# Optimization experiments

Measured on AMD Instinct MI355X. Metric: run time of the kernel, lower is better.

## Reference

```python
import jax, jax.numpy as jnp
import numpy as np

T, B, I, H = 1024, 64, 512, 512


def flip_batch(data, lengths):
    # data: [T, B, D]; reverse the first lengths[i] timesteps of each batch column i.
    t = jnp.arange(data.shape[0])[:, None]                 # [T, 1]
    L = lengths[None, :]                                   # [1, B]
    idx = jnp.where(t < L, L - 1 - t, t)                   # [T, B]
    return jnp.take_along_axis(data, idx[:, :, None], axis=0)


def lstm_scan(x, h0, c0, w_ih, w_hh, b):
    # x: [T, B, I]; standard torch LSTMCell math, gate order (i, f, g, o).
    def step(carry, xt):
        h, c = carry
        gates = xt @ w_ih.T + h @ w_hh.T + b               # [B, 4H]
        i, f, g, o = jnp.split(gates, 4, axis=-1)
        i = jax.nn.sigmoid(i)
        f = jax.nn.sigmoid(f)
        g = jnp.tanh(g)
        o = jax.nn.sigmoid(o)
        c = f * c + i * g
        h = o * jnp.tanh(c)
        return (h, c), h

    (_, _), ys = jax.lax.scan(step, (h0, c0), x)
    return ys                                              # [T, B, H]


def setup_inputs() -> dict:
    key = jax.random.key(0)
    ks = jax.random.split(key, 16)
    s = 0.05
    return {
        "input": jax.random.normal(ks[0], (T, B, I), jnp.float32),
        "lengths": jax.random.randint(ks[1], (B,), 0, T),
        "h0_f": jax.random.normal(ks[2], (B, H), jnp.float32) * s,
        "c0_f": jax.random.normal(ks[3], (B, H), jnp.float32) * s,
        "h0_b": jax.random.normal(ks[4], (B, H), jnp.float32) * s,
        "c0_b": jax.random.normal(ks[5], (B, H), jnp.float32) * s,
        "w_ih_f": jax.random.normal(ks[6], (4 * H, I), jnp.float32) * s,
        "w_hh_f": jax.random.normal(ks[7], (4 * H, H), jnp.float32) * s,
        "b_ih_f": jax.random.normal(ks[8], (4 * H,), jnp.float32) * s,
        "b_hh_f": jax.random.normal(ks[9], (4 * H,), jnp.float32) * s,
        "w_ih_b": jax.random.normal(ks[10], (4 * H, I), jnp.float32) * s,
        "w_hh_b": jax.random.normal(ks[11], (4 * H, H), jnp.float32) * s,
        "b_ih_b": jax.random.normal(ks[12], (4 * H,), jnp.float32) * s,
        "b_hh_b": jax.random.normal(ks[13], (4 * H,), jnp.float32) * s,
    }


def reference(input, lengths, h0_f, c0_f, h0_b, c0_b,
              w_ih_f, w_hh_f, b_ih_f, b_hh_f,
              w_ih_b, w_hh_b, b_ih_b, b_hh_b):
    # Forward-direction layer: plain left-to-right scan over full sequence.
    out_f = lstm_scan(input, h0_f, c0_f, w_ih_f, w_hh_f, b_ih_f + b_hh_f)
    # Backward layer with length-aware reversal (flipBatch), then flip outputs back.
    x_rev = flip_batch(input, lengths)
    ys = lstm_scan(x_rev, h0_b, c0_b, w_ih_b, w_hh_b, b_ih_b + b_hh_b)
    out_b = flip_batch(ys, lengths)
    # lengths provided => module returns (concat, None); return the output tensor.
    return jnp.concatenate([out_f, out_b], axis=-1)       # [T, B, 2H]
```

## Files before the change

kernel.cpp:

```cpp
#include <hip/hip_runtime.h>
#include <hip/hip_bf16.h>

#define T_LEN  1024
#define BATCH  64
#define HDIM   512
#define G4     2048

typedef __attribute__((ext_vector_type(8))) short short8;
typedef __attribute__((ext_vector_type(4))) float f32x4;
typedef __attribute__((ext_vector_type(4))) unsigned int u32x4;
typedef __hip_bfloat16 bf16;

__device__ __forceinline__ unsigned short bfbits(float f) {
    bf16 h = __float2bfloat16(f);
    return __builtin_bit_cast(unsigned short, h);
}
__device__ __forceinline__ float fsigmoid(float x) { return 1.f / (1.f + __expf(-x)); }
__device__ __forceinline__ float ftanh(float x)    { return 2.f / (1.f + __expf(-2.f * x)) - 1.f; }

__global__ void conv_weights(const float* __restrict__ wihf, const float* __restrict__ whhf,
                             const float* __restrict__ bihf, const float* __restrict__ bhhf,
                             const float* __restrict__ wihb, const float* __restrict__ whhb,
                             const float* __restrict__ bihb, const float* __restrict__ bhhb,
                             bf16* __restrict__ wih, bf16* __restrict__ whh,
                             float* __restrict__ bias)
{
    int i = blockIdx.x * 256 + threadIdx.x;
    const int n1 = G4 * HDIM;
    if (i < n1) {
        wih[i] = __float2bfloat16(wihf[i]);
        whh[i] = __float2bfloat16(whhf[i]);
    } else {
        int k = i - n1;
        wih[n1 + k] = __float2bfloat16(wihb[k]);
        whh[n1 + k] = __float2bfloat16(whhb[k]);
    }
    if (i < G4)          bias[i] = bihf[i] + bhhf[i];
    else if (i < 2 * G4) bias[i] = bihb[i - G4] + bhhb[i - G4];
}

__global__ void conv_x(const float* __restrict__ x, bf16* __restrict__ xb)
{
    size_t i = (size_t)blockIdx.x * 256 + threadIdx.x;
    const float* s = x + i * 8;
    float4 a = *reinterpret_cast<const float4*>(s);
    float4 b = *reinterpret_cast<const float4*>(s + 4);
    union { unsigned short us[8]; u32x4 v; } p;
    p.us[0] = bfbits(a.x); p.us[1] = bfbits(a.y); p.us[2] = bfbits(a.z); p.us[3] = bfbits(a.w);
    p.us[4] = bfbits(b.x); p.us[5] = bfbits(b.y); p.us[6] = bfbits(b.z); p.us[7] = bfbits(b.w);
    *reinterpret_cast<u32x4*>(xb + i * 8) = p.v;
}

__global__ void init_state(const float* __restrict__ h0f, const float* __restrict__ c0f,
                           const float* __restrict__ h0b, const float* __restrict__ c0b,
                           bf16* __restrict__ hbuf, float* __restrict__ cbuf,
                           unsigned* __restrict__ flags, unsigned* __restrict__ xcdarr,
                           unsigned* __restrict__ abortw)
{
    int i = blockIdx.x * 256 + threadIdx.x;
    int d = i >> 15, r = i & 32767;
    const float* h0 = d ? h0b : h0f;
    const float* c0 = d ? c0b : c0f;
    hbuf[(0 * 2 + d) * (BATCH * HDIM) + r] = __float2bfloat16(h0[r]);
    cbuf[d * (BATCH * HDIM) + r] = c0[r];
    if (blockIdx.x == 0) {
        flags[threadIdx.x]  = 0;
        xcdarr[threadIdx.x] = 0;
        if (threadIdx.x == 0) *abortw = 0;
    }
}

__global__ __launch_bounds__(256, 1) void lstm_full(
        const bf16* __restrict__ xb,
        const bf16* __restrict__ wih,
        const bf16* __restrict__ whh,
        const float* __restrict__ bias,
        const int*  __restrict__ lengths,
        bf16*       __restrict__ hbuf,
        float*      __restrict__ cbuf,
        float*      __restrict__ out,
        unsigned*   __restrict__ flags,
        unsigned*   __restrict__ xcdarr,
        unsigned*   __restrict__ abortw)
{
    __shared__ __align__(16) char Wl[64 * 2048];
    __shared__ __align__(16) char Al[16 * 1024];
    __shared__ float Gl[16][68];
    __shared__ int ok_sh;

    const int tid  = threadIdx.x;
    const int team = (int)blockIdx.x & 7;
    const int rank = (int)blockIdx.x >> 3;
    const int dir  = team >> 2;
    const int b0   = (team & 3) * 16;
    const int u0   = rank * 16;
    const int lane = tid & 63;
    const int w    = tid >> 6;

    if (tid == 0) {
        unsigned xcc;
        asm volatile("s_getreg_b32 %0, hwreg(20, 0, 32)" : "=s"(xcc));
        __hip_atomic_store(&xcdarr[blockIdx.x], (xcc & 0xFu) + 1u,
                           __ATOMIC_RELAXED, __HIP_MEMORY_SCOPE_SYSTEM);
    }

    {
        const bf16* wihd = wih + (size_t)dir * G4 * HDIM;
        const bf16* whhd = whh + (size_t)dir * G4 * HDIM;
#pragma unroll
        for (int i = 0; i < 32; i++) {
            int q = tid + i * 256;
            int c = q >> 7, s = q & 127;
            int grow = (c >> 4) * HDIM + u0 + (c & 15);
            const bf16* src = (s < 64) ? (wihd + (size_t)grow * HDIM + s * 8)
                                       : (whhd + (size_t)grow * HDIM + (s - 64) * 8);
            u32x4 v = *reinterpret_cast<const u32x4*>(src);
            *reinterpret_cast<u32x4*>(&Wl[(c * 2048 + s * 16) ^ ((c & 7) << 4)]) = v;
        }
    }

    if (rank == 0) {
        if (w == 0) {
            int idx = (lane < 32) ? (team + lane * 8) : ((team ^ 1) + (lane - 32) * 8);
            const unsigned* p = xcdarr + idx;
            unsigned v = 0, cnt = 0; int timeout = 0;
            for (;;) {
                v = __hip_atomic_load(p, __ATOMIC_RELAXED, __HIP_MEMORY_SCOPE_SYSTEM);
                if (__all((int)((v & 31u) != 0u))) break;
                if (++cnt > (1u << 20)) { timeout = 1; break; }
            }
            unsigned my = (unsigned)__shfl((int)(v & 31u), 0);
            int ok = (!timeout) &&
                     __all(lane < 32 ? (int)((v & 31u) == my) : (int)((v & 31u) != my));
            if (ok && lane < 32)
                __hip_atomic_store(&flags[team * 32 + lane], 0u,
                                   __ATOMIC_RELAXED, __HIP_MEMORY_SCOPE_WORKGROUP);
            asm volatile("s_waitcnt vmcnt(0)" ::: "memory");
            if (lane == 0) {
                unsigned pub = my | 32u | (ok ? 64u : 0u);
                __hip_atomic_store(&xcdarr[blockIdx.x], pub,
                                   __ATOMIC_RELAXED, __HIP_MEMORY_SCOPE_SYSTEM);
                ok_sh = ok;
            }
        }
    } else {
        if (tid == 0) {
            const unsigned* p = xcdarr + team;
            unsigned v;
            do {
                v = __hip_atomic_load(p, __ATOMIC_RELAXED, __HIP_MEMORY_SCOPE_SYSTEM);
            } while (!(v & 32u));
            ok_sh = (int)((v >> 6) & 1u);
        }
    }

    const int bb = tid >> 4;
    const int uu = tid & 15;
    const int b_glob = b0 + bb;
    const int Lb = lengths[b_glob];
    float c_reg = __hip_atomic_load(&cbuf[((size_t)dir * BATCH + b_glob) * HDIM + u0 + uu],
                                    __ATOMIC_RELAXED, __HIP_MEMORY_SCOPE_SYSTEM);
    float bias_r[4];
#pragma unroll
    for (int g = 0; g < 4; g++)
        bias_r[g] = bias[dir * G4 + g * HDIM + u0 + uu];
    int Lw[4];
#pragma unroll
    for (int i = 0; i < 4; i++) Lw[i] = lengths[b0 + i * 4 + w];

    const int arow  = lane & 15;
    const int axor  = (arow & 7) << 4;
    const int abase = arow * 1024;
    const int brow  = w * 16 + (lane & 15);
    const int bxor  = (brow & 7) << 4;
    const int bbase = brow * 2048;
    const int kbhi  = (lane >> 4) * 16;

    unsigned* flagw = flags + team * 32 + rank;
    const unsigned* pollp = flags + team * 32 + (lane & 31);

    __syncthreads();
    const bool fast = (ok_sh != 0);

    for (int t = 0; t < T_LEN; ++t) {
        const int p = t & 1;

#pragma unroll
        for (int i = 0; i < 4; i++) {
            int row = i * 4 + w;
            int st = t;
            if (dir) { int L = Lw[i]; st = (t < L) ? (L - 1 - t) : t; }
            u32x4 v = *reinterpret_cast<const u32x4*>(
                xb + ((size_t)st * BATCH + b0 + row) * HDIM + lane * 8);
            *reinterpret_cast<u32x4*>(&Al[(row * 1024 + lane * 16) ^ ((row & 7) << 4)]) = v;
        }
        __syncthreads();

        f32x4 acc = f32x4{0.f, 0.f, 0.f, 0.f};
#pragma unroll
        for (int ks = 0; ks < 16; ++ks) {
            int kb = ks * 64 + kbhi;
            short8 a = *reinterpret_cast<const short8*>(&Al[(abase + kb) ^ axor]);
            short8 b = *reinterpret_cast<const short8*>(&Wl[(bbase + kb) ^ bxor]);
            acc = __builtin_amdgcn_mfma_f32_16x16x32_bf16(a, b, acc, 0, 0, 0);
        }

        if (w == 0 && t > 0) {
            unsigned token = (unsigned)t, v, cnt = 0;
            if (fast) {
                for (;;) {
                    asm volatile("global_load_dword %0, %1, off sc0\n\ts_waitcnt vmcnt(0)"
                                 : "=v"(v) : "v"(pollp) : "memory");
                    if (__all((int)(v >= token))) break;
                    if (((++cnt) & 4095u) == 0) {
                        if (__hip_atomic_load(abortw, __ATOMIC_RELAXED, __HIP_MEMORY_SCOPE_SYSTEM)) break;
                        if (cnt > (1u << 22)) {
                            __hip_atomic_store(abortw, 1u, __ATOMIC_RELAXED, __HIP_MEMORY_SCOPE_SYSTEM);
                            break;
                        }
                    }
                }
            } else {
                for (;;) {
                    v = __hip_atomic_load(pollp, __ATOMIC_RELAXED, __HIP_MEMORY_SCOPE_SYSTEM);
                    if (__all((int)(v >= token))) break;
                    if (((++cnt) & 4095u) == 0) {
                        if (__hip_atomic_load(abortw, __ATOMIC_RELAXED, __HIP_MEMORY_SCOPE_SYSTEM)) break;
                        if (cnt > (1u << 22)) {
                            __hip_atomic_store(abortw, 1u, __ATOMIC_RELAXED, __HIP_MEMORY_SCOPE_SYSTEM);
                            break;
                        }
                    }
                }
            }
        }
        __syncthreads();

        {
            const bf16* hb = hbuf + ((size_t)(p * 2 + dir) * BATCH + b0) * HDIM;
            if (fast && t > 0) {
                u32x4 h4[4];
#pragma unroll
                for (int i = 0; i < 4; i++) {
                    int row = i * 4 + w;
                    const bf16* hp = hb + (size_t)row * HDIM + lane * 8;
                    asm volatile("global_load_dwordx4 %0, %1, off sc0"
                                 : "=v"(h4[i]) : "v"(hp) : "memory");
                }
                asm volatile("s_waitcnt vmcnt(0)" ::: "memory");
#pragma unroll
                for (int i = 0; i < 4; i++) {
                    int row = i * 4 + w;
                    *reinterpret_cast<u32x4*>(&Al[(row * 1024 + lane * 16) ^ ((row & 7) << 4)]) = h4[i];
                }
            } else {
#pragma unroll
                for (int i = 0; i < 8; i++) {
                    int q = tid + i * 256;
                    int row = q >> 7, sb = (q & 127) * 8;
                    unsigned long long v = __hip_atomic_load(
                        reinterpret_cast<const unsigned long long*>(hb) + q,
                        __ATOMIC_RELAXED, __HIP_MEMORY_SCOPE_SYSTEM);
                    *reinterpret_cast<unsigned long long*>(
                        &Al[(row * 1024 + sb) ^ ((row & 7) << 4)]) = v;
                }
            }
        }
        __syncthreads();

#pragma unroll
        for (int ks = 0; ks < 16; ++ks) {
            int kb = ks * 64 + kbhi;
            short8 a = *reinterpret_cast<const short8*>(&Al[(abase + kb) ^ axor]);
            short8 b = *reinterpret_cast<const short8*>(&Wl[(bbase + 1024 + kb) ^ bxor]);
            acc = __builtin_amdgcn_mfma_f32_16x16x32_bf16(a, b, acc, 0, 0, 0);
        }

        {
            int col = w * 16 + (lane & 15);
            int rb  = (lane >> 4) * 4;
#pragma unroll
            for (int r = 0; r < 4; r++) Gl[rb + r][col] = acc[r];
        }
        __syncthreads();

        float gi = Gl[bb][uu]      + bias_r[0];
        float gf = Gl[bb][16 + uu] + bias_r[1];
        float gg = Gl[bb][32 + uu] + bias_r[2];
        float go = Gl[bb][48 + uu] + bias_r[3];
        float iv = fsigmoid(gi), fv = fsigmoid(gf), gv = ftanh(gg), ov = fsigmoid(go);
        c_reg = fv * c_reg + iv * gv;
        float hv = ov * ftanh(c_reg);

        unsigned lo = (unsigned)bfbits(hv);
        unsigned hi = (unsigned)__shfl_down((int)lo, 1);
        if ((uu & 1) == 0) {
            unsigned* hw = reinterpret_cast<unsigned*>(
                hbuf + (size_t)((p ^ 1) * 2 + dir) * BATCH * HDIM) + ((b_glob * HDIM + u0 + uu) >> 1);
            unsigned val = lo | (hi << 16);
            if (fast) __hip_atomic_store(hw, val, __ATOMIC_RELAXED, __HIP_MEMORY_SCOPE_WORKGROUP);
            else      __hip_atomic_store(hw, val, __ATOMIC_RELAXED, __HIP_MEMORY_SCOPE_SYSTEM);
        }
        int tout = t;
        if (dir) tout = (t < Lb) ? (Lb - 1 - t) : t;
        out[((size_t)tout * BATCH + b_glob) * (2 * HDIM) + dir * HDIM + u0 + uu] = hv;

        __syncthreads();
        if (tid == 0) {
            unsigned tok = (unsigned)(t + 1);
            if (fast) __hip_atomic_store(flagw, tok, __ATOMIC_RELAXED, __HIP_MEMORY_SCOPE_WORKGROUP);
            else      __hip_atomic_store(flagw, tok, __ATOMIC_RELAXED, __HIP_MEMORY_SCOPE_SYSTEM);
        }
    }

    cbuf[((size_t)dir * BATCH + b_glob) * HDIM + u0 + uu] = c_reg;
}

extern "C" void kernel_launch(void* const* d_in, const int* in_sizes, int n_in,
                              void* d_out, int out_size, void* d_ws, size_t ws_size,
                              hipStream_t stream)
{
    const float* x     = (const float*)d_in[0];
    const int* lengths = (const int*)d_in[1];
    const float* h0f   = (const float*)d_in[2];
    const float* c0f   = (const float*)d_in[3];
    const float* h0b   = (const float*)d_in[4];
    const float* c0b   = (const float*)d_in[5];
    const float* wihf  = (const float*)d_in[6];
    const float* whhf  = (const float*)d_in[7];
    const float* bihf  = (const float*)d_in[8];
    const float* bhhf  = (const float*)d_in[9];
    const float* wihb  = (const float*)d_in[10];
    const float* whhb  = (const float*)d_in[11];
    const float* bihb  = (const float*)d_in[12];
    const float* bhhb  = (const float*)d_in[13];
    float* out = (float*)d_out;

    char* ws = (char*)d_ws;
    bf16*     wih_bf = (bf16*)(ws);
    bf16*     whh_bf = (bf16*)(ws + (4u << 20));
    float*    bias   = (float*)(ws + (8u << 20));
    bf16*     hbuf   = (bf16*)(ws + (9u << 20));
    float*    cbuf   = (float*)(ws + (10u << 20));
    unsigned* flags  = (unsigned*)(ws + (11u << 20));
    unsigned* xcdarr = (unsigned*)(ws + (11u << 20) + 4096);
    unsigned* abortw = (unsigned*)(ws + (11u << 20) + 8192);
    bf16*     xb     = (bf16*)(ws + (16u << 20));

    conv_weights<<<dim3(2 * G4 * HDIM / 256), dim3(256), 0, stream>>>(
        wihf, whhf, bihf, bhhf, wihb, whhb, bihb, bhhb, wih_bf, whh_bf, bias);
    conv_x<<<dim3((T_LEN * BATCH * HDIM / 8) / 256), dim3(256), 0, stream>>>(x, xb);
    init_state<<<dim3(2 * BATCH * HDIM / 256), dim3(256), 0, stream>>>(
        h0f, c0f, h0b, c0b, hbuf, cbuf, flags, xcdarr, abortw);

    lstm_full<<<dim3(256), dim3(256), 0, stream>>>(
        xb, wih_bf, whh_bf, bias, lengths, hbuf, cbuf, out, flags, xcdarr, abortw);
}
```

Before: 2.488 ms.

## Keep LSTM weights in registers and prefetch next-step inputs before the barrier

Each wave now holds its slices of the input and recurrent weights in VGPRs (short8 fragments) instead of staging them in LDS. It computes the input projection before polling for the previous hidden state, and loads h and x directly from global memory into MFMA operands instead of going through LDS. The next timestep's x is prefetched after the recurrent MFMAs, and the bias is folded into the accumulator init. h0/c0 are read directly, which removes the init_state kernel and the cbuf buffer. A 100KB LDS pad keeps one block per CU. The aim is to take LDS round-trips and a barrier off the serial recurrent critical path, at the cost of much higher register pressure.

Measured after the change: 4.543 ms. 1.83x slower.

```diff
diff --git a/kernel.cpp b/kernel.cpp
--- a/kernel.cpp
+++ b/kernel.cpp
@@ -51,23 +51,13 @@
     *reinterpret_cast<u32x4*>(xb + i * 8) = p.v;
 }
 
-__global__ void init_state(const float* __restrict__ h0f, const float* __restrict__ c0f,
-                           const float* __restrict__ h0b, const float* __restrict__ c0b,
-                           bf16* __restrict__ hbuf, float* __restrict__ cbuf,
-                           unsigned* __restrict__ flags, unsigned* __restrict__ xcdarr,
-                           unsigned* __restrict__ abortw)
-{
-    int i = blockIdx.x * 256 + threadIdx.x;
-    int d = i >> 15, r = i & 32767;
-    const float* h0 = d ? h0b : h0f;
-    const float* c0 = d ? c0b : c0f;
-    hbuf[(0 * 2 + d) * (BATCH * HDIM) + r] = __float2bfloat16(h0[r]);
-    cbuf[d * (BATCH * HDIM) + r] = c0[r];
-    if (blockIdx.x == 0) {
-        flags[threadIdx.x]  = 0;
-        xcdarr[threadIdx.x] = 0;
-        if (threadIdx.x == 0) *abortw = 0;
-    }
+__global__ void init_sync(unsigned* __restrict__ flags, unsigned* __restrict__ xcdarr,
+                          unsigned* __restrict__ abortw)
+{
+    int i = threadIdx.x;
+    __hip_atomic_store(&flags[i],  0u, __ATOMIC_RELAXED, __HIP_MEMORY_SCOPE_SYSTEM);
+    __hip_atomic_store(&xcdarr[i], 0u, __ATOMIC_RELAXED, __HIP_MEMORY_SCOPE_SYSTEM);
+    if (i == 0) __hip_atomic_store(abortw, 0u, __ATOMIC_RELAXED, __HIP_MEMORY_SCOPE_SYSTEM);
 }
 
 __global__ __launch_bounds__(256, 1) void lstm_full(
@@ -76,17 +66,17 @@
         const bf16* __restrict__ whh,
         const float* __restrict__ bias,
         const int*  __restrict__ lengths,
+        const float* __restrict__ h0f, const float* __restrict__ c0f,
+        const float* __restrict__ h0b, const float* __restrict__ c0b,
         bf16*       __restrict__ hbuf,
-        float*      __restrict__ cbuf,
         float*      __restrict__ out,
         unsigned*   __restrict__ flags,
         unsigned*   __restrict__ xcdarr,
         unsigned*   __restrict__ abortw)
 {
-    __shared__ __align__(16) char Wl[64 * 2048];
-    __shared__ __align__(16) char Al[16 * 1024];
     __shared__ float Gl[16][68];
     __shared__ int ok_sh;
+    __shared__ char lds_pad[100000];
 
     const int tid  = threadIdx.x;
     const int team = (int)blockIdx.x & 7;
@@ -96,27 +86,16 @@
     const int u0   = rank * 16;
     const int lane = tid & 63;
     const int w    = tid >> 6;
+    const int uu   = lane & 15;
+    const int q    = lane >> 4;
+
+    ((volatile char*)lds_pad)[tid] = 1;
 
     if (tid == 0) {
         unsigned xcc;
         asm volatile("s_getreg_b32 %0, hwreg(20, 0, 32)" : "=s"(xcc));
         __hip_atomic_store(&xcdarr[blockIdx.x], (xcc & 0xFu) + 1u,
                            __ATOMIC_RELAXED, __HIP_MEMORY_SCOPE_SYSTEM);
-    }
-
-    {
-        const bf16* wihd = wih + (size_t)dir * G4 * HDIM;
-        const bf16* whhd = whh + (size_t)dir * G4 * HDIM;
-#pragma unroll
-        for (int i = 0; i < 32; i++) {
-            int q = tid + i * 256;
-            int c = q >> 7, s = q & 127;
-            int grow = (c >> 4) * HDIM + u0 + (c & 15);
-            const bf16* src = (s < 64) ? (wihd + (size_t)grow * HDIM + s * 8)
-                                       : (whhd + (size_t)grow * HDIM + (s - 64) * 8);
-            u32x4 v = *reinterpret_cast<const u32x4*>(src);
-            *reinterpret_cast<u32x4*>(&Wl[(c * 2048 + s * 16) ^ ((c & 7) << 4)]) = v;
-        }
     }
 
     if (rank == 0) {
@@ -132,9 +111,11 @@
             unsigned my = (unsigned)__shfl((int)(v & 31u), 0);
             int ok = (!timeout) &&
                      __all(lane < 32 ? (int)((v & 31u) == my) : (int)((v & 31u) != my));
-            if (ok && lane < 32)
-                __hip_atomic_store(&flags[team * 32 + lane], 0u,
+            if (ok && lane < 32) {
+                unsigned old = __hip_atomic_exchange(&flags[team * 32 + lane], 0u,
                                    __ATOMIC_RELAXED, __HIP_MEMORY_SCOPE_WORKGROUP);
+                (void)old;
+            }
             asm volatile("s_waitcnt vmcnt(0)" ::: "memory");
             if (lane == 0) {
                 unsigned pub = my | 32u | (ok ? 64u : 0u);
@@ -146,66 +127,63 @@
     } else {
         if (tid == 0) {
             const unsigned* p = xcdarr + team;
-            unsigned v;
-            do {
+            unsigned v, cnt = 0;
+            for (;;) {
                 v = __hip_atomic_load(p, __ATOMIC_RELAXED, __HIP_MEMORY_SCOPE_SYSTEM);
-            } while (!(v & 32u));
+                if (v & 32u) break;
+                if (++cnt > (1u << 24)) { v = 32u; break; }
+            }
             ok_sh = (int)((v >> 6) & 1u);
         }
     }
 
+    short8 BI[16], BH[16];
+    {
+        const size_t grow = (size_t)(w * HDIM + u0 + uu);
+        const bf16* wi = wih + (size_t)dir * G4 * HDIM + grow * HDIM + q * 8;
+        const bf16* wh = whh + (size_t)dir * G4 * HDIM + grow * HDIM + q * 8;
+#pragma unroll
+        for (int ks = 0; ks < 16; ++ks) {
+            BI[ks] = *reinterpret_cast<const short8*>(wi + ks * 32);
+            BH[ks] = *reinterpret_cast<const short8*>(wh + ks * 32);
+        }
+    }
+    const float bs = bias[dir * G4 + w * HDIM + u0 + uu];
+
     const int bb = tid >> 4;
-    const int uu = tid & 15;
+    const int cu = tid & 15;
     const int b_glob = b0 + bb;
     const int Lb = lengths[b_glob];
-    float c_reg = __hip_atomic_load(&cbuf[((size_t)dir * BATCH + b_glob) * HDIM + u0 + uu],
-                                    __ATOMIC_RELAXED, __HIP_MEMORY_SCOPE_SYSTEM);
-    float bias_r[4];
-#pragma unroll
-    for (int g = 0; g < 4; g++)
-        bias_r[g] = bias[dir * G4 + g * HDIM + u0 + uu];
-    int Lw[4];
-#pragma unroll
-    for (int i = 0; i < 4; i++) Lw[i] = lengths[b0 + i * 4 + w];
-
-    const int arow  = lane & 15;
-    const int axor  = (arow & 7) << 4;
-    const int abase = arow * 1024;
-    const int brow  = w * 16 + (lane & 15);
-    const int bxor  = (brow & 7) << 4;
-    const int bbase = brow * 2048;
-    const int kbhi  = (lane >> 4) * 16;
-
+    float c_reg = (dir ? c0b : c0f)[(size_t)b_glob * HDIM + u0 + cu];
+
+    const int LA = lengths[b0 + uu];
+
+    const unsigned* pollp = flags + team * 32 + (lane & 31);
     unsigned* flagw = flags + team * 32 + rank;
-    const unsigned* pollp = flags + team * 32 + (lane & 31);
 
     __syncthreads();
     const bool fast = (ok_sh != 0);
+    int dead = 0;
+
+    u32x4 A[16];
+    {
+        int st = 0; if (dir) st = (0 < LA) ? (LA - 1) : 0;
+        const bf16* xp = xb + ((size_t)st * BATCH + b0 + uu) * HDIM + q * 8;
+#pragma unroll
+        for (int ks = 0; ks < 16; ++ks)
+            A[ks] = *reinterpret_cast<const u32x4*>(xp + ks * 32);
+    }
 
     for (int t = 0; t < T_LEN; ++t) {
         const int p = t & 1;
 
-#pragma unroll
-        for (int i = 0; i < 4; i++) {
-            int row = i * 4 + w;
-            int st = t;
-            if (dir) { int L = Lw[i]; st = (t < L) ? (L - 1 - t) : t; }
-            u32x4 v = *reinterpret_cast<const u32x4*>(
-                xb + ((size_t)st * BATCH + b0 + row) * HDIM + lane * 8);
-            *reinterpret_cast<u32x4*>(&Al[(row * 1024 + lane * 16) ^ ((row & 7) << 4)]) = v;
-        }
-        __syncthreads();
-
-        f32x4 acc = f32x4{0.f, 0.f, 0.f, 0.f};
-#pragma unroll
-        for (int ks = 0; ks < 16; ++ks) {
-            int kb = ks * 64 + kbhi;
-            short8 a = *reinterpret_cast<const short8*>(&Al[(abase + kb) ^ axor]);
-            short8 b = *reinterpret_cast<const short8*>(&Wl[(bbase + kb) ^ bxor]);
-            acc = __builtin_amdgcn_mfma_f32_16x16x32_bf16(a, b, acc, 0, 0, 0);
-        }
-
-        if (w == 0 && t > 0) {
+        f32x4 accx = f32x4{bs, bs, bs, bs};
+#pragma unroll
+        for (int ks = 0; ks < 16; ++ks)
+            accx = __builtin_amdgcn_mfma_f32_16x16x32_bf16(
+                __builtin_bit_cast(short8, A[ks]), BI[ks], accx, 0, 0, 0);
+
+        if (w == 0 && t > 0 && !dead) {
             unsigned token = (unsigned)t, v, cnt = 0;
             if (fast) {
                 for (;;) {
@@ -213,10 +191,10 @@
                                  : "=v"(v) : "v"(pollp) : "memory");
                     if (__all((int)(v >= token))) break;
                     if (((++cnt) & 4095u) == 0) {
-                        if (__hip_atomic_load(abortw, __ATOMIC_RELAXED, __HIP_MEMORY_SCOPE_SYSTEM)) break;
+                        if (__hip_atomic_load(abortw, __ATOMIC_RELAXED, __HIP_MEMORY_SCOPE_SYSTEM)) { dead = 1; break; }
                         if (cnt > (1u << 22)) {
                             __hip_atomic_store(abortw, 1u, __ATOMIC_RELAXED, __HIP_MEMORY_SCOPE_SYSTEM);
-                            break;
+                            dead = 1; break;
                         }
                     }
                 }
@@ -225,10 +203,10 @@
                     v = __hip_atomic_load(pollp, __ATOMIC_RELAXED, __HIP_MEMORY_SCOPE_SYSTEM);
                     if (__all((int)(v >= token))) break;
                     if (((++cnt) & 4095u) == 0) {
-                        if (__hip_atomic_load(abortw, __ATOMIC_RELAXED, __HIP_MEMORY_SCOPE_SYSTEM)) break;
+                        if (__hip_atomic_load(abortw, __ATOMIC_RELAXED, __HIP_MEMORY_SCOPE_SYSTEM)) { dead = 1; break; }
                         if (cnt > (1u << 22)) {
                             __hip_atomic_store(abortw, 1u, __ATOMIC_RELAXED, __HIP_MEMORY_SCOPE_SYSTEM);
-                            break;
+                            dead = 1; break;
                         }
                     }
                 }
@@ -236,84 +214,111 @@
         }
         __syncthreads();
 
+        u32x4 H[16];
+        if (t == 0) {
+            const float* h0p = (dir ? h0b : h0f) + (size_t)(b0 + uu) * HDIM;
+#pragma unroll
+            for (int ks = 0; ks < 16; ++ks) {
+                const float* s = h0p + ks * 32 + q * 8;
+                float4 f0 = *reinterpret_cast<const float4*>(s);
+                float4 f1 = *reinterpret_cast<const float4*>(s + 4);
+                union { unsigned short us[8]; u32x4 v; } pk;
+                pk.us[0] = bfbits(f0.x); pk.us[1] = bfbits(f0.y);
+                pk.us[2] = bfbits(f0.z); pk.us[3] = bfbits(f0.w);
+                pk.us[4] = bfbits(f1.x); pk.us[5] = bfbits(f1.y);
+                pk.us[6] = bfbits(f1.z); pk.us[7] = bfbits(f1.w);
+                H[ks] = pk.v;
+            }
+        } else {
+            const bf16* hb = hbuf + (size_t)(p * 2 + dir) * (BATCH * HDIM)
+                                  + (size_t)(b0 + uu) * HDIM + q * 8;
+            if (fast) {
+#pragma unroll
+                for (int ks = 0; ks < 16; ++ks)
+                    asm volatile("global_load_dwordx4 %0, %1, off sc0"
+                                 : "=v"(H[ks]) : "v"(hb + ks * 32) : "memory");
+                asm volatile("s_waitcnt vmcnt(0)" ::: "memory");
+                __builtin_amdgcn_sched_barrier(0);
+            } else {
+#pragma unroll
+                for (int ks = 0; ks < 16; ++ks) {
+                    union { unsigned long long qv[2]; u32x4 v; } pk;
+                    pk.qv[0] = __hip_atomic_load(
+                        reinterpret_cast<const unsigned long long*>(hb + ks * 32),
+                        __ATOMIC_RELAXED, __HIP_MEMORY_SCOPE_SYSTEM);
+                    pk.qv[1] = __hip_atomic_load(
+                        reinterpret_cast<const unsigned long long*>(hb + ks * 32 + 4),
+                        __ATOMIC_RELAXED, __HIP_MEMORY_SCOPE_SYSTEM);
+                    H[ks] = pk.v;
+                }
+            }
+        }
+
+        f32x4 acch0 = f32x4{0.f, 0.f, 0.f, 0.f};
+        f32x4 acch1 = f32x4{0.f, 0.f, 0.f, 0.f};
+#pragma unroll
+        for (int ks = 0; ks < 8; ++ks) {
+            acch0 = __builtin_amdgcn_mfma_f32_16x16x32_bf16(
+                __builtin_bit_cast(short8, H[2 * ks]),     BH[2 * ks],     acch0, 0, 0, 0);
+            acch1 = __builtin_amdgcn_mfma_f32_16x16x32_bf16(
+                __builtin_bit_cast(short8, H[2 * ks + 1]), BH[2 * ks + 1], acch1, 0, 0, 0);
+        }
+
+        if (t + 1 < T_LEN) {
+            int tn = t + 1, st = tn;
+            if (dir) st = (tn < LA) ? (LA - 1 - tn) : tn;
+            const bf16* xp = xb + ((size_t)st * BATCH + b0 + uu) * HDIM + q * 8;
+#pragma unroll
+            for (int ks = 0; ks < 16; ++ks)
+                A[ks] = *reinterpret_cast<const u32x4*>(xp + ks * 32);
+        }
+
         {
-            const bf16* hb = hbuf + ((size_t)(p * 2 + dir) * BATCH + b0) * HDIM;
-            if (fast && t > 0) {
-                u32x4 h4[4];
-#pragma unroll
-                for (int i = 0; i < 4; i++) {
-                    int row = i * 4 + w;
-                    const bf16* hp = hb + (size_t)row * HDIM + lane * 8;
-                    asm volatile("global_load_dwordx4 %0, %1, off sc0"
-                                 : "=v"(h4[i]) : "v"(hp) : "memory");
-                }
-                asm volatile("s_waitcnt vmcnt(0)" ::: "memory");
-#pragma unroll
-                for (int i = 0; i < 4; i++) {
-                    int row = i * 4 + w;
-                    *reinterpret_cast<u32x4*>(&Al[(row * 1024 + lane * 16) ^ ((row & 7) << 4)]) = h4[i];
-                }
-            } else {
-#pragma unroll
-                for (int i = 0; i < 8; i++) {
-                    int q = tid + i * 256;
-                    int row = q >> 7, sb = (q & 127) * 8;
-                    unsigned long long v = __hip_atomic_load(
-                        reinterpret_cast<const unsigned long long*>(hb) + q,
-                        __ATOMIC_RELAXED, __HIP_MEMORY_SCOPE_SYSTEM);
-                    *reinterpret_cast<unsigned long long*>(
-                        &Al[(row * 1024 + sb) ^ ((row & 7) << 4)]) = v;
-                }
-            }
+            int col = w * 16 + uu;
+#pragma unroll
+            for (int r = 0; r < 4; ++r)
+                Gl[q * 4 + r][col] = accx[r] + acch0[r] + acch1[r];
         }
         __syncthreads();
 
-#pragma unroll
-        for (int ks = 0; ks < 16; ++ks) {
-            int kb = ks * 64 + kbhi;
-            short8 a = *reinterpret_cast<const short8*>(&Al[(abase + kb) ^ axor]);
-            short8 b = *reinterpret_cast<const short8*>(&Wl[(bbase + 1024 + kb) ^ bxor]);
-            acc = __builtin_amdgcn_mfma_f32_16x16x32_bf16(a, b, acc, 0, 0, 0);
-        }
-
-        {
-            int col = w * 16 + (lane & 15);
-            int rb  = (lane >> 4) * 4;
-#pragma unroll
-            for (int r = 0; r < 4; r++) Gl[rb + r][col] = acc[r];
-        }
-        __syncthreads();
-
-        float gi = Gl[bb][uu]      + bias_r[0];
-        float gf = Gl[bb][16 + uu] + bias_r[1];
-        float gg = Gl[bb][32 + uu] + bias_r[2];
-        float go = Gl[bb][48 + uu] + bias_r[3];
+        float gi = Gl[bb][cu];
+        float gf = Gl[bb][16 + cu];
+        float gg = Gl[bb][32 + cu];
+        float go = Gl[bb][48 + cu];
         float iv = fsigmoid(gi), fv = fsigmoid(gf), gv = ftanh(gg), ov = fsigmoid(go);
         c_reg = fv * c_reg + iv * gv;
         float hv = ov * ftanh(c_reg);
 
+        bf16* hd = hbuf + (size_t)((p ^ 1) * 2 + dir) * (BATCH * HDIM);
         unsigned lo = (unsigned)bfbits(hv);
         unsigned hi = (unsigned)__shfl_down((int)lo, 1);
-        if ((uu & 1) == 0) {
-            unsigned* hw = reinterpret_cast<unsigned*>(
-                hbuf + (size_t)((p ^ 1) * 2 + dir) * BATCH * HDIM) + ((b_glob * HDIM + u0 + uu) >> 1);
+        if ((cu & 1) == 0) {
+            unsigned* hw = reinterpret_cast<unsigned*>(hd) + ((b_glob * HDIM + u0 + cu) >> 1);
             unsigned val = lo | (hi << 16);
-            if (fast) __hip_atomic_store(hw, val, __ATOMIC_RELAXED, __HIP_MEMORY_SCOPE_WORKGROUP);
-            else      __hip_atomic_store(hw, val, __ATOMIC_RELAXED, __HIP_MEMORY_SCOPE_SYSTEM);
+            if (fast) {
+                unsigned old = __hip_atomic_exchange(hw, val, __ATOMIC_RELAXED,
+                                                     __HIP_MEMORY_SCOPE_WORKGROUP);
+                (void)old;
+            } else {
+                __hip_atomic_store(hw, val, __ATOMIC_RELAXED, __HIP_MEMORY_SCOPE_SYSTEM);
+            }
         }
         int tout = t;
         if (dir) tout = (t < Lb) ? (Lb - 1 - t) : t;
-        out[((size_t)tout * BATCH + b_glob) * (2 * HDIM) + dir * HDIM + u0 + uu] = hv;
+        out[((size_t)tout * BATCH + b_glob) * (2 * HDIM) + dir * HDIM + u0 + cu] = hv;
 
         __syncthreads();
         if (tid == 0) {
             unsigned tok = (unsigned)(t + 1);
-            if (fast) __hip_atomic_store(flagw, tok, __ATOMIC_RELAXED, __HIP_MEMORY_SCOPE_WORKGROUP);
-            else      __hip_atomic_store(flagw, tok, __ATOMIC_RELAXED, __HIP_MEMORY_SCOPE_SYSTEM);
-        }
-    }
-
-    cbuf[((size_t)dir * BATCH + b_glob) * HDIM + u0 + uu] = c_reg;
+            if (fast) {
+                unsigned old = __hip_atomic_exchange(flagw, tok, __ATOMIC_RELAXED,
+                                                     __HIP_MEMORY_SCOPE_WORKGROUP);
+                (void)old;
+            } else {
+                __hip_atomic_store(flagw, tok, __ATOMIC_RELAXED, __HIP_MEMORY_SCOPE_SYSTEM);
+            }
+        }
+    }
 }
 
 extern "C" void kernel_launch(void* const* d_in, const int* in_sizes, int n_in,
@@ -341,7 +346,6 @@
     bf16*     whh_bf = (bf16*)(ws + (4u << 20));
     float*    bias   = (float*)(ws + (8u << 20));
     bf16*     hbuf   = (bf16*)(ws + (9u << 20));
-    float*    cbuf   = (float*)(ws + (10u << 20));
     unsigned* flags  = (unsigned*)(ws + (11u << 20));
     unsigned* xcdarr = (unsigned*)(ws + (11u << 20) + 4096);
     unsigned* abortw = (unsigned*)(ws + (11u << 20) + 8192);
@@ -350,9 +354,9 @@
     conv_weights<<<dim3(2 * G4 * HDIM / 256), dim3(256), 0, stream>>>(
         wihf, whhf, bihf, bhhf, wihb, whhb, bihb, bhhb, wih_bf, whh_bf, bias);
     conv_x<<<dim3((T_LEN * BATCH * HDIM / 8) / 256), dim3(256), 0, stream>>>(x, xb);
-    init_state<<<dim3(2 * BATCH * HDIM / 256), dim3(256), 0, stream>>>(
-        h0f, c0f, h0b, c0b, hbuf, cbuf, flags, xcdarr, abortw);
+    init_sync<<<dim3(1), dim3(256), 0, stream>>>(flags, xcdarr, abortw);
 
     lstm_full<<<dim3(256), dim3(256), 0, stream>>>(
-        xb, wih_bf, whh_bf, bias, lengths, hbuf, cbuf, out, flags, xcdarr, abortw);
-}
+        xb, wih_bf, whh_bf, bias, lengths, h0f, c0f, h0b, c0b,
+        hbuf, out, flags, xcdarr, abortw);
+}
```
